# Optimization experiments

Hardware: AMD Instinct MI355X
Metric: run time of the kernel (lower is better)

Reference implementation:

```python
import jax, jax.numpy as jnp
from jax import lax
import numpy as np

BN_EPS = 1e-5

def nearest_resize(x, out_h, out_w):
    # torch F.interpolate(mode='nearest'): src = floor(dst * in / out)
    B, C, H, W = x.shape
    hi = (jnp.arange(out_h) * H) // out_h
    wi = (jnp.arange(out_w) * W) // out_w
    return x[:, :, hi][:, :, :, wi]

def conv1x1(x, w, b=None):
    y = jnp.einsum('bchw,oc->bohw', x, w)
    if b is not None:
        y = y + b[None, :, None, None]
    return y

def dwconv(x, w, stride, pad):
    C = x.shape[1]
    return lax.conv_general_dilated(x, w, (stride, stride), [(pad, pad), (pad, pad)],
                                    dimension_numbers=('NCHW', 'OIHW', 'NCHW'),
                                    feature_group_count=C)

def bn(x, g, b, m, v):
    scale = g / jnp.sqrt(v + BN_EPS)
    return (x - m[None, :, None, None]) * scale[None, :, None, None] + b[None, :, None, None]


def setup_inputs() -> dict:
    key = jax.random.key(0)
    ks = jax.random.split(key, 8)
    B, C, H0, W0 = 4, 512, 192, 192
    w_scale = 0.05
    return {
        'x': jax.random.normal(ks[0], (B, C, H0, W0), jnp.float32),
        'q_w': jax.random.normal(ks[1], (C, C), jnp.float32) * w_scale,
        'q_b': jnp.zeros((C,), jnp.float32),
        'kv_w': jax.random.normal(ks[2], (2 * C, C), jnp.float32) * w_scale,
        'kv_b': jnp.zeros((2 * C,), jnp.float32),
        'sr1_w': jax.random.normal(ks[3], (C, 1, 2, 2), jnp.float32) * w_scale,
        'bn1_g': jnp.ones((C,), jnp.float32),
        'bn1_b': jnp.zeros((C,), jnp.float32),
        'bn1_m': jnp.zeros((C,), jnp.float32),
        'bn1_v': jnp.ones((C,), jnp.float32),
        'sr2_w': jax.random.normal(ks[4], (C, C), jnp.float32) * w_scale,
        'bn2_g': jnp.ones((C,), jnp.float32),
        'bn2_b': jnp.zeros((C,), jnp.float32),
        'bn2_m': jnp.zeros((C,), jnp.float32),
        'bn2_v': jnp.ones((C,), jnp.float32),
        'lc_w': jax.random.normal(ks[5], (C, 1, 3, 3), jnp.float32) * w_scale,
        'lc_b': jnp.zeros((C,), jnp.float32),
        'head_num': 8,
    }


def reference(x, q_w, q_b, kv_w, kv_b, sr1_w, bn1_g, bn1_b, bn1_m, bn1_v,
              sr2_w, bn2_g, bn2_b, bn2_m, bn2_v, lc_w, lc_b, head_num):
    origin_h, origin_w = x.shape[2], x.shape[3]
    x = nearest_resize(x, origin_h // 4, origin_w // 4)
    B, C, H, W = x.shape
    hd = C // head_num
    scale = hd ** (-0.5)

    # q projection (1x1 conv with bias)
    q = conv1x1(x, q_w, q_b)  # [B,C,H,W]

    # spatial reduction: depthwise conv(k=sr, s=sr, p=sr//2) + BN + ReLU, then 1x1 + BN
    sr = sr1_w.shape[-1]
    kv = jax.nn.relu(bn(dwconv(x, sr1_w, sr, sr // 2), bn1_g, bn1_b, bn1_m, bn1_v))
    kv = bn(conv1x1(kv, sr2_w), bn2_g, bn2_b, bn2_m, bn2_v)

    # local depthwise 3x3 conv residual
    kv = dwconv(kv, lc_w, 1, 1) + lc_b[None, :, None, None] + kv

    # kv projection (1x1 conv, 2C output)
    kv = conv1x1(kv, kv_w, kv_b)
    k, v = jnp.split(kv, 2, axis=1)  # each [B,C,Hs,Ws]
    M = k.shape[2] * k.shape[3]

    q_ = jnp.swapaxes(q.reshape(B, head_num, hd, H * W), -1, -2)  # [B,h,N,hd]
    k_ = k.reshape(B, head_num, hd, M)                             # [B,h,hd,M]
    v_ = jnp.swapaxes(v.reshape(B, head_num, hd, M), -1, -2)       # [B,h,M,hd]

    attn = jax.nn.softmax(jnp.matmul(q_, k_) * scale, axis=-1)     # [B,h,N,M]
    out = jnp.swapaxes(jnp.matmul(attn, v_), -1, -2).reshape(B, C, H, W)

    # NOTE: original torch code passes size=(origin_w, origin_h)
    out = nearest_resize(out, origin_w, origin_h)
    return out
```

## Files before the change

### kernel.cpp

```cpp
#include <hip/hip_runtime.h>

#define Bsz 4
#define Cc  512
#define C2  1024
#define H0c 192
#define Hh  48
#define Nn  2304
#define HNh 8
#define HD  64
#define Hs  25
#define Ms  625

typedef const float* fp;
typedef _Float16 f16;
typedef __attribute__((ext_vector_type(8))) _Float16 f16x8;
typedef __attribute__((ext_vector_type(4))) _Float16 f16x4;
typedef __attribute__((ext_vector_type(4))) float    f32x4;

__global__ __launch_bounds__(256) void k_cvtw(fp __restrict__ q_w, fp __restrict__ sr2_w,
                                              fp __restrict__ kv_w, f16* __restrict__ wh) {
    int idx = blockIdx.x * 256 + threadIdx.x;
    float v;
    if (idx < 262144)      v = q_w[idx];
    else if (idx < 524288) v = sr2_w[idx - 262144];
    else                   v = kv_w[idx - 524288];
    wh[idx] = (f16)v;
}

__global__ __launch_bounds__(256) void k_ds_t(fp __restrict__ x,
                                              float* __restrict__ xds,
                                              f16* __restrict__ xt) {
    __shared__ float tile[32][33];
    const int b = blockIdx.z;
    const int s0 = blockIdx.x * 32, r0 = blockIdx.y * 32;
    const int t = threadIdx.x;
    const float* xb = x + (size_t)b * Cc * H0c * H0c;
    float* xdsb = xds + (size_t)b * Cc * Nn;
    #pragma unroll
    for (int p = 0; p < 4; p++) {
        int e = t + p * 256; int i = e >> 5, j = e & 31;
        int c = r0 + i, n = s0 + j;
        float v = xb[((size_t)c * H0c + (n / Hh) * 4) * H0c + (n % Hh) * 4];
        tile[i][j] = v;
        xdsb[(size_t)c * Nn + n] = v;
    }
    __syncthreads();
    #pragma unroll
    for (int p = 0; p < 4; p++) {
        int e = t + p * 256; int oi = e >> 5, oj = e & 31;
        xt[((size_t)b * Nn + s0 + oi) * Cc + r0 + oj] = (f16)tile[oj][oi];
    }
}

__global__ __launch_bounds__(256) void k_sr1t(const float* __restrict__ xds,
                                              fp __restrict__ w, fp g, fp bb, fp bm, fp bv,
                                              f16* __restrict__ kv1t) {
    __shared__ float tile[32][33];
    const int b = blockIdx.z;
    const int s0 = blockIdx.x * 32, r0 = blockIdx.y * 32;
    const int t = threadIdx.x;
    #pragma unroll
    for (int p = 0; p < 4; p++) {
        int e = t + p * 256; int i = e >> 5, j = e & 31;
        int c = r0 + i, n = s0 + j;
        float v = 0.f;
        if (n < Ms) {
            int ho = n / Hs, wo = n % Hs;
            const float* src = xds + ((size_t)b * Cc + c) * Nn;
            float acc = 0.f;
            #pragma unroll
            for (int di = 0; di < 2; di++) {
                int ih = ho * 2 - 1 + di;
                if (ih < 0 || ih >= Hh) continue;
                #pragma unroll
                for (int dj = 0; dj < 2; dj++) {
                    int iw = wo * 2 - 1 + dj;
                    if (iw < 0 || iw >= Hh) continue;
                    acc += w[c * 4 + di * 2 + dj] * src[ih * Hh + iw];
                }
            }
            float sc = g[c] * rsqrtf(bv[c] + 1e-5f);
            v = fmaxf((acc - bm[c]) * sc + bb[c], 0.f);
        }
        tile[i][j] = v;
    }
    __syncthreads();
    #pragma unroll
    for (int p = 0; p < 4; p++) {
        int e = t + p * 256; int oi = e >> 5, oj = e & 31;
        if (s0 + oi < Ms)
            kv1t[((size_t)b * Ms + s0 + oi) * Cc + r0 + oj] = (f16)tile[oj][oi];
    }
}

__global__ __launch_bounds__(256) void k_lct(const float* __restrict__ kv2,
                                             fp __restrict__ w, fp __restrict__ lb,
                                             f16* __restrict__ kv3t) {
    __shared__ float tile[32][33];
    const int b = blockIdx.z;
    const int s0 = blockIdx.x * 32, r0 = blockIdx.y * 32;
    const int t = threadIdx.x;
    #pragma unroll
    for (int p = 0; p < 4; p++) {
        int e = t + p * 256; int i = e >> 5, j = e & 31;
        int c = r0 + i, n = s0 + j;
        float v = 0.f;
        if (n < Ms) {
            int ho = n / Hs, wo = n % Hs;
            const float* src = kv2 + ((size_t)b * Cc + c) * Ms;
            float acc = 0.f;
            #pragma unroll
            for (int di = 0; di < 3; di++) {
                int ih = ho - 1 + di;
                if (ih < 0 || ih >= Hs) continue;
                #pragma unroll
                for (int dj = 0; dj < 3; dj++) {
                    int iw = wo - 1 + dj;
                    if (iw < 0 || iw >= Hs) continue;
                    acc += w[c * 9 + di * 3 + dj] * src[ih * Hs + iw];
                }
            }
            v = acc + lb[c] + src[n];
        }
        tile[i][j] = v;
    }
    __syncthreads();
    #pragma unroll
    for (int p = 0; p < 4; p++) {
        int e = t + p * 256; int oi = e >> 5, oj = e & 31;
        if (s0 + oi < Ms)
            kv3t[((size_t)b * Ms + s0 + oi) * Cc + r0 + oj] = (f16)tile[oj][oi];
    }
}

__global__ __launch_bounds__(256) void k_gemm_mfma(
    const f16* __restrict__ W, const f16* __restrict__ Xt,
    float* __restrict__ Yf, f16* __restrict__ Yt, f16* __restrict__ Vt,
    const int Md, const int Nd, const int NtRows, const int mode, const float oscale,
    fp __restrict__ bias,
    fp __restrict__ bn_g, fp __restrict__ bn_b, fp __restrict__ bn_m, fp __restrict__ bn_v)
{
    __shared__ f16 sA[128 * 80];
    __shared__ f16 sB[128 * 80];
    const int b  = blockIdx.z;
    const int m0 = blockIdx.y * 128, n0 = blockIdx.x * 128;
    const int t = threadIdx.x;
    const int lane = t & 63, w = t >> 6;
    const int lm = lane & 15, q = lane >> 4;
    const int wm = w >> 1, wn = w & 1;
    const f16* Xb = Xt + (size_t)b * Nd * 512;

    f32x4 acc[4][4];
    #pragma unroll
    for (int i = 0; i < 4; i++)
        #pragma unroll
        for (int j = 0; j < 4; j++)
            #pragma unroll
            for (int r = 0; r < 4; r++) acc[i][j][r] = 0.f;

    for (int k0 = 0; k0 < 512; k0 += 64) {
        {
            int r = t >> 1, hh = (t & 1) * 32;
            const f16* wr = W + (size_t)(m0 + r) * 512 + k0 + hh;
            f16* dst = &sA[r * 80 + hh];
            #pragma unroll
            for (int i = 0; i < 4; i++)
                *(f16x8*)&dst[i * 8] = *(const f16x8*)&wr[i * 8];
        }
        {
            int r = t >> 1, hh = (t & 1) * 32;
            bool ok = (n0 + r) < Nd;
            const f16* xr = Xb + (size_t)(n0 + r) * 512 + k0 + hh;
            f16* dst = &sB[r * 80 + hh];
            #pragma unroll
            for (int i = 0; i < 4; i++) {
                f16x8 v;
                if (ok) {
                    v = *(const f16x8*)&xr[i * 8];
                } else {
                    for (int z = 0; z < 8; z++) v[z] = (f16)0.f;
                }
                *(f16x8*)&dst[i * 8] = v;
            }
        }
        __syncthreads();
        #pragma unroll
        for (int ks = 0; ks < 2; ks++) {
            f16x8 af[4], bf[4];
            #pragma unroll
            for (int i = 0; i < 4; i++)
                af[i] = *(const f16x8*)&sA[(wm * 64 + i * 16 + lm) * 80 + ks * 32 + q * 8];
            #pragma unroll
            for (int j = 0; j < 4; j++)
                bf[j] = *(const f16x8*)&sB[(wn * 64 + j * 16 + lm) * 80 + ks * 32 + q * 8];
            #pragma unroll
            for (int i = 0; i < 4; i++)
                #pragma unroll
                for (int j = 0; j < 4; j++)
                    acc[i][j] = __builtin_amdgcn_mfma_f32_16x16x32_f16(af[i], bf[j], acc[i][j], 0, 0, 0);
        }
        __syncthreads();
    }

    #pragma unroll
    for (int i = 0; i < 4; i++) {
        int ob = m0 + wm * 64 + i * 16 + q * 4;
        float badd[4], bsc[4], bsh[4];
        #pragma unroll
        for (int r = 0; r < 4; r++) {
            int o = ob + r;
            badd[r] = bias ? bias[o] : 0.f;
            if (bn_g) { bsc[r] = bn_g[o] * rsqrtf(bn_v[o] + 1e-5f); bsh[r] = bn_b[o] - bn_m[o] * bsc[r]; }
            else      { bsc[r] = 1.f; bsh[r] = 0.f; }
        }
        #pragma unroll
        for (int j = 0; j < 4; j++) {
            int n = n0 + wn * 64 + j * 16 + lm;
            f32x4 a = acc[i][j];
            if (mode == 0) {
                if (n < Nd) {
                    #pragma unroll
                    for (int r = 0; r < 4; r++)
                        Yf[((size_t)b * Md + ob + r) * Nd + n] = (a[r] + badd[r]) * bsc[r] + bsh[r];
                }
            } else if (mode == 1 || (mode == 2 && ob < 512)) {
                f16x4 h;
                #pragma unroll
                for (int r = 0; r < 4; r++) h[r] = (f16)((a[r] + badd[r]) * oscale);
                int hh = ob >> 6, d0 = ob & 63;
                *(f16x4*)&Yt[((size_t)(b * 8 + hh) * NtRows + n) * 64 + d0] = h;
            } else {
                #pragma unroll
                for (int r = 0; r < 4; r++) {
                    float val = (n < Nd) ? (a[r] + badd[r]) : 0.f;
                    Vt[((size_t)b * Cc + (ob + r - 512)) * 640 + n] = (f16)val;
                }
            }
        }
    }
}

__global__ __launch_bounds__(256) void k_attn_mfma(
    const f16* __restrict__ Qt, const f16* __restrict__ Kt,
    const f16* __restrict__ Vt, float* __restrict__ Obuf)
{
    __shared__ f16 sK[64 * 80];
    __shared__ f16 sV[64 * 80];
    __shared__ f16 sP[4][16 * 80];

    int bh = blockIdx.y;
    int n0 = blockIdx.x * 64;
    int t = threadIdx.x, w = t >> 6, lane = t & 63;
    int lm = lane & 15, q = lane >> 4;
    f16* sPw = &sP[w][0];

    f16x8 qf[2];
    {
        const f16* qrow = Qt + ((size_t)bh * Nn + n0 + w * 16 + lm) * 64;
        qf[0] = *(const f16x8*)&qrow[q * 8];
        qf[1] = *(const f16x8*)&qrow[32 + q * 8];
    }

    f32x4 od[4];
    #pragma unroll
    for (int dt = 0; dt < 4; dt++)
        #pragma unroll
        for (int r = 0; r < 4; r++) od[dt][r] = 0.f;
    float mold[4], lold[4];
    #pragma unroll
    for (int r = 0; r < 4; r++) { mold[r] = -1e30f; lold[r] = 0.f; }

    int kr = t >> 2, kc = t & 3;
    const f16* kbase = Kt + (size_t)bh * 640 * 64;
    const f16* vbase = Vt + (size_t)bh * 64 * 640;

    for (int mc = 0; mc < 640; mc += 64) {
        {
            const f16* ksrc = kbase + (size_t)(mc + kr) * 64;
            *(f16x8*)&sK[kr * 80 + kc * 8]      = *(const f16x8*)&ksrc[kc * 8];
            *(f16x8*)&sK[kr * 80 + 32 + kc * 8] = *(const f16x8*)&ksrc[32 + kc * 8];
            const f16* vsrc = vbase + (size_t)kr * 640 + mc;
            *(f16x8*)&sV[kr * 80 + kc * 8]      = *(const f16x8*)&vsrc[kc * 8];
            *(f16x8*)&sV[kr * 80 + 32 + kc * 8] = *(const f16x8*)&vsrc[32 + kc * 8];
        }
        __syncthreads();

        f32x4 sc4[4];
        #pragma unroll
        for (int j = 0; j < 4; j++)
            #pragma unroll
            for (int r = 0; r < 4; r++) sc4[j][r] = 0.f;
        #pragma unroll
        for (int ks = 0; ks < 2; ks++) {
            #pragma unroll
            for (int j = 0; j < 4; j++) {
                f16x8 kf = *(const f16x8*)&sK[(j * 16 + lm) * 80 + ks * 32 + q * 8];
                sc4[j] = __builtin_amdgcn_mfma_f32_16x16x32_f16(qf[ks], kf, sc4[j], 0, 0, 0);
            }
        }

        const bool lastc = (mc >= 576);
        #pragma unroll
        for (int reg = 0; reg < 4; reg++) {
            float mx;
            if (lastc) {
                mx = -1e30f;
                #pragma unroll
                for (int j = 0; j < 4; j++) {
                    float s = sc4[j][reg];
                    if (576 + j * 16 + lm >= Ms) s = -1e30f;
                    sc4[j][reg] = s;
                    mx = fmaxf(mx, s);
                }
            } else {
                mx = fmaxf(fmaxf(sc4[0][reg], sc4[1][reg]),
                           fmaxf(sc4[2][reg], sc4[3][reg]));
            }
            #pragma unroll
            for (int off = 1; off < 16; off <<= 1) mx = fmaxf(mx, __shfl_xor(mx, off));
            float mnew = fmaxf(mold[reg], mx);
            float alpha = __expf(mold[reg] - mnew);
            float rs = 0.f;
            #pragma unroll
            for (int j = 0; j < 4; j++) {
                float p = __expf(sc4[j][reg] - mnew);
                sc4[j][reg] = p;
                rs += p;
            }
            #pragma unroll
            for (int off = 1; off < 16; off <<= 1) rs += __shfl_xor(rs, off);
            lold[reg] = lold[reg] * alpha + rs;
            mold[reg] = mnew;
            #pragma unroll
            for (int dt = 0; dt < 4; dt++) od[dt][reg] *= alpha;
            #pragma unroll
            for (int j = 0; j < 4; j++)
                sPw[(q * 4 + reg) * 80 + j * 16 + lm] = (f16)sc4[j][reg];
        }

        #pragma unroll
        for (int ks = 0; ks < 2; ks++) {
            f16x8 pa = *(const f16x8*)&sPw[lm * 80 + ks * 32 + q * 8];
            #pragma unroll
            for (int dt = 0; dt < 4; dt++) {
                f16x8 vf = *(const f16x8*)&sV[(dt * 16 + lm) * 80 + ks * 32 + q * 8];
                od[dt] = __builtin_amdgcn_mfma_f32_16x16x32_f16(pa, vf, od[dt], 0, 0, 0);
            }
        }
        __syncthreads();
    }

    float inv[4];
    #pragma unroll
    for (int r = 0; r < 4; r++) inv[r] = 1.f / lold[r];
    #pragma unroll
    for (int dt = 0; dt < 4; dt++) {
        f32x4 o;
        #pragma unroll
        for (int r = 0; r < 4; r++) o[r] = od[dt][r] * inv[r];
        size_t c = (size_t)bh * 64 + dt * 16 + lm;
        *(f32x4*)&Obuf[c * Nn + n0 + w * 16 + q * 4] = o;
    }
}

__global__ __launch_bounds__(256) void k_upsample(const float* __restrict__ O,
                                                  float* __restrict__ out) {
    size_t idx = (size_t)blockIdx.x * 256 + threadIdx.x;
    if (idx >= (size_t)Bsz * Cc * H0c * 48) return;
    int jg = (int)(idx % 48);
    int i  = (int)((idx / 48) % H0c);
    int bc = (int)(idx / ((size_t)48 * H0c));
    float s = O[(size_t)bc * Nn + (i >> 2) * Hh + jg];
    float4 pack = make_float4(s, s, s, s);
    *(float4*)(out + ((size_t)bc * H0c + i) * H0c + jg * 4) = pack;
}

extern "C" void kernel_launch(void* const* d_in, const int* in_sizes, int n_in,
                              void* d_out, int out_size, void* d_ws, size_t ws_size,
                              hipStream_t stream) {
    (void)in_sizes; (void)n_in; (void)out_size; (void)ws_size;
    fp x     = (fp)d_in[0];
    fp q_w   = (fp)d_in[1];
    fp q_b   = (fp)d_in[2];
    fp kv_w  = (fp)d_in[3];
    fp kv_b  = (fp)d_in[4];
    fp sr1_w = (fp)d_in[5];
    fp bn1_g = (fp)d_in[6];
    fp bn1_b = (fp)d_in[7];
    fp bn1_m = (fp)d_in[8];
    fp bn1_v = (fp)d_in[9];
    fp sr2_w = (fp)d_in[10];
    fp bn2_g = (fp)d_in[11];
    fp bn2_b = (fp)d_in[12];
    fp bn2_m = (fp)d_in[13];
    fp bn2_v = (fp)d_in[14];
    fp lc_w  = (fp)d_in[15];
    fp lc_b  = (fp)d_in[16];
    float* out = (float*)d_out;

    float* ws   = (float*)d_ws;
    float* xds  = ws;
    float* Obuf = ws;
    float* kv2  = ws + 4718592;
    f16*   Kt   = (f16*)(ws + 5998592);
    f16*   vt   = (f16*)(ws + 6653952);
    f16*   xt   = (f16*)(ws + 7309312);
    f16*   kv1t = xt;
    f16*   kv3t = xt;
    f16*   Qt   = (f16*)(ws + 9668608);
    f16*   wh   = (f16*)(ws + 12027904);

    k_cvtw<<<4096, 256, 0, stream>>>(q_w, sr2_w, kv_w, wh);
    k_ds_t<<<dim3(72, 16, Bsz), 256, 0, stream>>>(x, xds, xt);
    k_gemm_mfma<<<dim3(18, 4, Bsz), 256, 0, stream>>>(wh, xt, nullptr, Qt, nullptr,
        Cc, Nn, Nn, 1, 0.125f, q_b, nullptr, nullptr, nullptr, nullptr);
    k_sr1t<<<dim3(20, 16, Bsz), 256, 0, stream>>>(xds, sr1_w, bn1_g, bn1_b, bn1_m, bn1_v, kv1t);
    k_gemm_mfma<<<dim3(5, 4, Bsz), 256, 0, stream>>>(wh + 262144, kv1t, kv2, nullptr, nullptr,
        Cc, Ms, 0, 0, 1.f, nullptr, bn2_g, bn2_b, bn2_m, bn2_v);
    k_lct<<<dim3(20, 16, Bsz), 256, 0, stream>>>(kv2, lc_w, lc_b, kv3t);
    k_gemm_mfma<<<dim3(5, 8, Bsz), 256, 0, stream>>>(wh + 524288, kv3t, nullptr, Kt, vt,
        C2, Ms, 640, 2, 1.f, kv_b, nullptr, nullptr, nullptr, nullptr);
    k_attn_mfma<<<dim3(Nn / 64, Bsz * HNh), 256, 0, stream>>>(Qt, Kt, vt, Obuf);
    k_upsample<<<(unsigned)((size_t)Bsz * Cc * H0c * 48 / 256), 256, 0, stream>>>(Obuf, out);
}
```

Measured before the change: 617.2 us.

## Merge front-end kernels and co-launch Q and SR2 GEMMs, drop xds buffer

Three kernels become one launch: the weight fp16 conversion (now float4-vectorized), the downsample-transpose, and the SR1 depthwise+BN+ReLU. SR1 now reads directly from the strided full-resolution x, so the fp32 downsampled intermediate no longer needs to be written and read back. The Q projection GEMM and the SR2 GEMM are fused into a single launch with a flattened block index, so the small SR2 GEMM overlaps the larger one. The upsample kernel becomes a grid-stride loop over 2048 blocks, and the workspace is relaid out because kv1t no longer aliases xt. The SR1 path's strided gathers from x may be less cache-friendly than reading the compact intermediate.

```diff
diff --git a/kernel.cpp b/kernel.cpp
--- a/kernel.cpp
+++ b/kernel.cpp
@@ -17,79 +17,81 @@
 typedef __attribute__((ext_vector_type(4))) _Float16 f16x4;
 typedef __attribute__((ext_vector_type(4))) float    f32x4;
 
-__global__ __launch_bounds__(256) void k_cvtw(fp __restrict__ q_w, fp __restrict__ sr2_w,
-                                              fp __restrict__ kv_w, f16* __restrict__ wh) {
-    int idx = blockIdx.x * 256 + threadIdx.x;
-    float v;
-    if (idx < 262144)      v = q_w[idx];
-    else if (idx < 524288) v = sr2_w[idx - 262144];
-    else                   v = kv_w[idx - 524288];
-    wh[idx] = (f16)v;
-}
-
-__global__ __launch_bounds__(256) void k_ds_t(fp __restrict__ x,
-                                              float* __restrict__ xds,
-                                              f16* __restrict__ xt) {
+__global__ __launch_bounds__(256) void k_front(
+    fp __restrict__ x, f16* __restrict__ xt, f16* __restrict__ kv1t,
+    fp __restrict__ w1, fp g, fp bb, fp bm, fp bv,
+    fp __restrict__ q_w, fp __restrict__ sr2_w, fp __restrict__ kv_w,
+    f16* __restrict__ wh)
+{
     __shared__ float tile[32][33];
-    const int b = blockIdx.z;
-    const int s0 = blockIdx.x * 32, r0 = blockIdx.y * 32;
     const int t = threadIdx.x;
-    const float* xb = x + (size_t)b * Cc * H0c * H0c;
-    float* xdsb = xds + (size_t)b * Cc * Nn;
-    #pragma unroll
-    for (int p = 0; p < 4; p++) {
-        int e = t + p * 256; int i = e >> 5, j = e & 31;
-        int c = r0 + i, n = s0 + j;
-        float v = xb[((size_t)c * H0c + (n / Hh) * 4) * H0c + (n % Hh) * 4];
-        tile[i][j] = v;
-        xdsb[(size_t)c * Nn + n] = v;
-    }
-    __syncthreads();
-    #pragma unroll
-    for (int p = 0; p < 4; p++) {
-        int e = t + p * 256; int oi = e >> 5, oj = e & 31;
-        xt[((size_t)b * Nn + s0 + oi) * Cc + r0 + oj] = (f16)tile[oj][oi];
-    }
-}
-
-__global__ __launch_bounds__(256) void k_sr1t(const float* __restrict__ xds,
-                                              fp __restrict__ w, fp g, fp bb, fp bm, fp bv,
-                                              f16* __restrict__ kv1t) {
-    __shared__ float tile[32][33];
-    const int b = blockIdx.z;
-    const int s0 = blockIdx.x * 32, r0 = blockIdx.y * 32;
-    const int t = threadIdx.x;
-    #pragma unroll
-    for (int p = 0; p < 4; p++) {
-        int e = t + p * 256; int i = e >> 5, j = e & 31;
-        int c = r0 + i, n = s0 + j;
-        float v = 0.f;
-        if (n < Ms) {
-            int ho = n / Hs, wo = n % Hs;
-            const float* src = xds + ((size_t)b * Cc + c) * Nn;
-            float acc = 0.f;
-            #pragma unroll
-            for (int di = 0; di < 2; di++) {
-                int ih = ho * 2 - 1 + di;
-                if (ih < 0 || ih >= Hh) continue;
-                #pragma unroll
-                for (int dj = 0; dj < 2; dj++) {
-                    int iw = wo * 2 - 1 + dj;
-                    if (iw < 0 || iw >= Hh) continue;
-                    acc += w[c * 4 + di * 2 + dj] * src[ih * Hh + iw];
-                }
-            }
-            float sc = g[c] * rsqrtf(bv[c] + 1e-5f);
-            v = fmaxf((acc - bm[c]) * sc + bb[c], 0.f);
-        }
-        tile[i][j] = v;
-    }
-    __syncthreads();
-    #pragma unroll
-    for (int p = 0; p < 4; p++) {
-        int e = t + p * 256; int oi = e >> 5, oj = e & 31;
-        if (s0 + oi < Ms)
-            kv1t[((size_t)b * Ms + s0 + oi) * Cc + r0 + oj] = (f16)tile[oj][oi];
+    int bid = blockIdx.x;
+
+    if (bid < 4608) {
+        const int b  = bid / 1152;
+        const int yi = (bid / 72) % 16;
+        const int xi = bid % 72;
+        const int s0 = xi * 32, r0 = yi * 32;
+        const float* xb = x + (size_t)b * Cc * H0c * H0c;
+        #pragma unroll
+        for (int p = 0; p < 4; p++) {
+            int e = t + p * 256; int i = e >> 5, j = e & 31;
+            int c = r0 + i, n = s0 + j;
+            tile[i][j] = xb[((size_t)c * H0c + (n / Hh) * 4) * H0c + (n % Hh) * 4];
+        }
+        __syncthreads();
+        #pragma unroll
+        for (int p = 0; p < 4; p++) {
+            int e = t + p * 256; int oi = e >> 5, oj = e & 31;
+            xt[((size_t)b * Nn + s0 + oi) * Cc + r0 + oj] = (f16)tile[oj][oi];
+        }
+    } else if (bid < 5888) {
+        bid -= 4608;
+        const int b  = bid / 320;
+        const int yi = (bid / 20) % 16;
+        const int xi = bid % 20;
+        const int s0 = xi * 32, r0 = yi * 32;
+        #pragma unroll
+        for (int p = 0; p < 4; p++) {
+            int e = t + p * 256; int i = e >> 5, j = e & 31;
+            int c = r0 + i, n = s0 + j;
+            float v = 0.f;
+            if (n < Ms) {
+                int ho = n / Hs, wo = n % Hs;
+                const float* src = x + (size_t)(b * Cc + c) * H0c * H0c;
+                float acc = 0.f;
+                #pragma unroll
+                for (int di = 0; di < 2; di++) {
+                    int ih = ho * 2 - 1 + di;
+                    if (ih < 0 || ih >= Hh) continue;
+                    #pragma unroll
+                    for (int dj = 0; dj < 2; dj++) {
+                        int iw = wo * 2 - 1 + dj;
+                        if (iw < 0 || iw >= Hh) continue;
+                        acc += w1[c * 4 + di * 2 + dj] * src[(size_t)(ih * 4) * H0c + iw * 4];
+                    }
+                }
+                float sc = g[c] * rsqrtf(bv[c] + 1e-5f);
+                v = fmaxf((acc - bm[c]) * sc + bb[c], 0.f);
+            }
+            tile[i][j] = v;
+        }
+        __syncthreads();
+        #pragma unroll
+        for (int p = 0; p < 4; p++) {
+            int e = t + p * 256; int oi = e >> 5, oj = e & 31;
+            if (s0 + oi < Ms)
+                kv1t[((size_t)b * Ms + s0 + oi) * Cc + r0 + oj] = (f16)tile[oj][oi];
+        }
+    } else {
+        bid -= 5888;
+        int i4 = (bid * 256 + t) * 4;
+        float4 v;
+        if (i4 < 262144)      v = *(const float4*)&q_w[i4];
+        else if (i4 < 524288) v = *(const float4*)&sr2_w[i4 - 262144];
+        else                  v = *(const float4*)&kv_w[i4 - 524288];
+        f16x4 h; h[0] = (f16)v.x; h[1] = (f16)v.y; h[2] = (f16)v.z; h[3] = (f16)v.w;
+        *(f16x4*)&wh[i4] = h;
     }
 }
 
@@ -130,6 +132,112 @@
         int e = t + p * 256; int oi = e >> 5, oj = e & 31;
         if (s0 + oi < Ms)
             kv3t[((size_t)b * Ms + s0 + oi) * Cc + r0 + oj] = (f16)tile[oj][oi];
+    }
+}
+
+__device__ __forceinline__ void gemm_body(
+    const f16* __restrict__ W, const f16* __restrict__ Xt,
+    float* __restrict__ Yf, f16* __restrict__ Yt, f16* __restrict__ Vt,
+    const int Md, const int Nd, const int NtRows, const int mode, const float oscale,
+    fp __restrict__ bias,
+    fp __restrict__ bn_g, fp __restrict__ bn_b, fp __restrict__ bn_m, fp __restrict__ bn_v,
+    const int bx, const int by, const int bz, f16* sA, f16* sB)
+{
+    const int b  = bz;
+    const int m0 = by * 128, n0 = bx * 128;
+    const int t = threadIdx.x;
+    const int lane = t & 63, w = t >> 6;
+    const int lm = lane & 15, q = lane >> 4;
+    const int wm = w >> 1, wn = w & 1;
+    const f16* Xb = Xt + (size_t)b * Nd * 512;
+
+    f32x4 acc[4][4];
+    #pragma unroll
+    for (int i = 0; i < 4; i++)
+        #pragma unroll
+        for (int j = 0; j < 4; j++)
+            #pragma unroll
+            for (int r = 0; r < 4; r++) acc[i][j][r] = 0.f;
+
+    for (int k0 = 0; k0 < 512; k0 += 64) {
+        {
+            int r = t >> 1, hh = (t & 1) * 32;
+            const f16* wr = W + (size_t)(m0 + r) * 512 + k0 + hh;
+            f16* dst = &sA[r * 80 + hh];
+            #pragma unroll
+            for (int i = 0; i < 4; i++)
+                *(f16x8*)&dst[i * 8] = *(const f16x8*)&wr[i * 8];
+        }
+        {
+            int r = t >> 1, hh = (t & 1) * 32;
+            bool ok = (n0 + r) < Nd;
+            const f16* xr = Xb + (size_t)(n0 + r) * 512 + k0 + hh;
+            f16* dst = &sB[r * 80 + hh];
+            #pragma unroll
+            for (int i = 0; i < 4; i++) {
+                f16x8 v;
+                if (ok) {
+                    v = *(const f16x8*)&xr[i * 8];
+                } else {
+                    for (int z = 0; z < 8; z++) v[z] = (f16)0.f;
+                }
+                *(f16x8*)&dst[i * 8] = v;
+            }
+        }
+        __syncthreads();
+        #pragma unroll
+        for (int ks = 0; ks < 2; ks++) {
+            f16x8 af[4], bf[4];
+            #pragma unroll
+            for (int i = 0; i < 4; i++)
+                af[i] = *(const f16x8*)&sA[(wm * 64 + i * 16 + lm) * 80 + ks * 32 + q * 8];
+            #pragma unroll
+            for (int j = 0; j < 4; j++)
+                bf[j] = *(const f16x8*)&sB[(wn * 64 + j * 16 + lm) * 80 + ks * 32 + q * 8];
+            #pragma unroll
+            for (int i = 0; i < 4; i++)
+                #pragma unroll
+                for (int j = 0; j < 4; j++)
+                    acc[i][j] = __builtin_amdgcn_mfma_f32_16x16x32_f16(af[i], bf[j], acc[i][j], 0, 0, 0);
+        }
+        __syncthreads();
+    }
+
+    #pragma unroll
+    for (int i = 0; i < 4; i++) {
+        int ob = m0 + wm * 64 + i * 16 + q * 4;
+        float badd[4], bsc[4], bsh[4];
+        #pragma unroll
+        for (int r = 0; r < 4; r++) {
+            int o = ob + r;
+            badd[r] = bias ? bias[o] : 0.f;
+            if (bn_g) { bsc[r] = bn_g[o] * rsqrtf(bn_v[o] + 1e-5f); bsh[r] = bn_b[o] - bn_m[o] * bsc[r]; }
+            else      { bsc[r] = 1.f; bsh[r] = 0.f; }
+        }
+        #pragma unroll
+        for (int j = 0; j < 4; j++) {
+            int n = n0 + wn * 64 + j * 16 + lm;
+            f32x4 a = acc[i][j];
+            if (mode == 0) {
+                if (n < Nd) {
+                    #pragma unroll
+                    for (int r = 0; r < 4; r++)
+                        Yf[((size_t)b * Md + ob + r) * Nd + n] = (a[r] + badd[r]) * bsc[r] + bsh[r];
+                }
+            } else if (mode == 1 || (mode == 2 && ob < 512)) {
+                f16x4 h;
+                #pragma unroll
+                for (int r = 0; r < 4; r++) h[r] = (f16)((a[r] + badd[r]) * oscale);
+                int hh = ob >> 6, d0 = ob & 63;
+                *(f16x4*)&Yt[((size_t)(b * 8 + hh) * NtRows + n) * 64 + d0] = h;
+            } else {
+                #pragma unroll
+                for (int r = 0; r < 4; r++) {
+                    float val = (n < Nd) ? (a[r] + badd[r]) : 0.f;
+                    Vt[((size_t)b * Cc + (ob + r - 512)) * 640 + n] = (f16)val;
+                }
+            }
+        }
     }
 }
 
@@ -142,101 +250,29 @@
 {
     __shared__ f16 sA[128 * 80];
     __shared__ f16 sB[128 * 80];
-    const int b  = blockIdx.z;
-    const int m0 = blockIdx.y * 128, n0 = blockIdx.x * 128;
-    const int t = threadIdx.x;
-    const int lane = t & 63, w = t >> 6;
-    const int lm = lane & 15, q = lane >> 4;
-    const int wm = w >> 1, wn = w & 1;
-    const f16* Xb = Xt + (size_t)b * Nd * 512;
-
-    f32x4 acc[4][4];
-    #pragma unroll
-    for (int i = 0; i < 4; i++)
-        #pragma unroll
-        for (int j = 0; j < 4; j++)
-            #pragma unroll
-            for (int r = 0; r < 4; r++) acc[i][j][r] = 0.f;
-
-    for (int k0 = 0; k0 < 512; k0 += 64) {
-        {
-            int r = t >> 1, hh = (t & 1) * 32;
-            const f16* wr = W + (size_t)(m0 + r) * 512 + k0 + hh;
-            f16* dst = &sA[r * 80 + hh];
-            #pragma unroll
-            for (int i = 0; i < 4; i++)
-                *(f16x8*)&dst[i * 8] = *(const f16x8*)&wr[i * 8];
-        }
-        {
-            int r = t >> 1, hh = (t & 1) * 32;
-            bool ok = (n0 + r) < Nd;
-            const f16* xr = Xb + (size_t)(n0 + r) * 512 + k0 + hh;
-            f16* dst = &sB[r * 80 + hh];
-            #pragma unroll
-            for (int i = 0; i < 4; i++) {
-                f16x8 v;
-                if (ok) {
-                    v = *(const f16x8*)&xr[i * 8];
-                } else {
-                    for (int z = 0; z < 8; z++) v[z] = (f16)0.f;
-                }
-                *(f16x8*)&dst[i * 8] = v;
-            }
-        }
-        __syncthreads();
-        #pragma unroll
-        for (int ks = 0; ks < 2; ks++) {
-            f16x8 af[4], bf[4];
-            #pragma unroll
-            for (int i = 0; i < 4; i++)
-                af[i] = *(const f16x8*)&sA[(wm * 64 + i * 16 + lm) * 80 + ks * 32 + q * 8];
-            #pragma unroll
-            for (int j = 0; j < 4; j++)
-                bf[j] = *(const f16x8*)&sB[(wn * 64 + j * 16 + lm) * 80 + ks * 32 + q * 8];
-            #pragma unroll
-            for (int i = 0; i < 4; i++)
-                #pragma unroll
-                for (int j = 0; j < 4; j++)
-                    acc[i][j] = __builtin_amdgcn_mfma_f32_16x16x32_f16(af[i], bf[j], acc[i][j], 0, 0, 0);
-        }
-        __syncthreads();
-    }
-
-    #pragma unroll
-    for (int i = 0; i < 4; i++) {
-        int ob = m0 + wm * 64 + i * 16 + q * 4;
-        float badd[4], bsc[4], bsh[4];
-        #pragma unroll
-        for (int r = 0; r < 4; r++) {
-            int o = ob + r;
-            badd[r] = bias ? bias[o] : 0.f;
-            if (bn_g) { bsc[r] = bn_g[o] * rsqrtf(bn_v[o] + 1e-5f); bsh[r] = bn_b[o] - bn_m[o] * bsc[r]; }
-            else      { bsc[r] = 1.f; bsh[r] = 0.f; }
-        }
-        #pragma unroll
-        for (int j = 0; j < 4; j++) {
-            int n = n0 + wn * 64 + j * 16 + lm;
-            f32x4 a = acc[i][j];
-            if (mode == 0) {
-                if (n < Nd) {
-                    #pragma unroll
-                    for (int r = 0; r < 4; r++)
-                        Yf[((size_t)b * Md + ob + r) * Nd + n] = (a[r] + badd[r]) * bsc[r] + bsh[r];
-                }
-            } else if (mode == 1 || (mode == 2 && ob < 512)) {
-                f16x4 h;
-                #pragma unroll
-                for (int r = 0; r < 4; r++) h[r] = (f16)((a[r] + badd[r]) * oscale);
-                int hh = ob >> 6, d0 = ob & 63;
-                *(f16x4*)&Yt[((size_t)(b * 8 + hh) * NtRows + n) * 64 + d0] = h;
-            } else {
-                #pragma unroll
-                for (int r = 0; r < 4; r++) {
-                    float val = (n < Nd) ? (a[r] + badd[r]) : 0.f;
-                    Vt[((size_t)b * Cc + (ob + r - 512)) * 640 + n] = (f16)val;
-                }
-            }
-        }
+    gemm_body(W, Xt, Yf, Yt, Vt, Md, Nd, NtRows, mode, oscale,
+              bias, bn_g, bn_b, bn_m, bn_v,
+              blockIdx.x, blockIdx.y, blockIdx.z, sA, sB);
+}
+
+__global__ __launch_bounds__(256) void k_gemm2(
+    const f16* __restrict__ W0, const f16* __restrict__ X0, f16* __restrict__ Yt0,
+    const float osc0, fp __restrict__ bias0,
+    const f16* __restrict__ W1, const f16* __restrict__ X1, float* __restrict__ Yf1,
+    fp g1, fp b1, fp m1, fp v1)
+{
+    __shared__ f16 sA[128 * 80];
+    __shared__ f16 sB[128 * 80];
+    int bid = blockIdx.x;
+    if (bid < 288) {
+        int bx = bid % 18, by = (bid / 18) % 4, bz = bid / 72;
+        gemm_body(W0, X0, nullptr, Yt0, nullptr, Cc, Nn, Nn, 1, osc0,
+                  bias0, nullptr, nullptr, nullptr, nullptr, bx, by, bz, sA, sB);
+    } else {
+        bid -= 288;
+        int bx = bid % 5, by = (bid / 5) % 4, bz = bid / 20;
+        gemm_body(W1, X1, Yf1, nullptr, nullptr, Cc, Ms, 0, 0, 1.f,
+                  nullptr, g1, b1, m1, v1, bx, by, bz, sA, sB);
     }
 }
 
@@ -365,14 +401,16 @@
 
 __global__ __launch_bounds__(256) void k_upsample(const float* __restrict__ O,
                                                   float* __restrict__ out) {
-    size_t idx = (size_t)blockIdx.x * 256 + threadIdx.x;
-    if (idx >= (size_t)Bsz * Cc * H0c * 48) return;
-    int jg = (int)(idx % 48);
-    int i  = (int)((idx / 48) % H0c);
-    int bc = (int)(idx / ((size_t)48 * H0c));
-    float s = O[(size_t)bc * Nn + (i >> 2) * Hh + jg];
-    float4 pack = make_float4(s, s, s, s);
-    *(float4*)(out + ((size_t)bc * H0c + i) * H0c + jg * 4) = pack;
+    const size_t total = (size_t)Bsz * Cc * H0c * 48;
+    for (size_t idx = (size_t)blockIdx.x * 256 + threadIdx.x; idx < total;
+         idx += (size_t)gridDim.x * 256) {
+        int jg = (int)(idx % 48);
+        int i  = (int)((idx / 48) % H0c);
+        int bc = (int)(idx / ((size_t)48 * H0c));
+        float s = O[(size_t)bc * Nn + (i >> 2) * Hh + jg];
+        float4 pack = make_float4(s, s, s, s);
+        *(float4*)(out + ((size_t)bc * H0c + i) * H0c + jg * 4) = pack;
+    }
 }
 
 extern "C" void kernel_launch(void* const* d_in, const int* in_sizes, int n_in,
@@ -399,27 +437,23 @@
     float* out = (float*)d_out;
 
     float* ws   = (float*)d_ws;
-    float* xds  = ws;
+    f16*   xt   = (f16*)ws;
+    f16*   kv1t = (f16*)(ws + 2359296);
+    f16*   wh   = (f16*)(ws + 2999296);
+    float* kv2  = ws + 3523584;
     float* Obuf = ws;
-    float* kv2  = ws + 4718592;
-    f16*   Kt   = (f16*)(ws + 5998592);
-    f16*   vt   = (f16*)(ws + 6653952);
-    f16*   xt   = (f16*)(ws + 7309312);
-    f16*   kv1t = xt;
-    f16*   kv3t = xt;
-    f16*   Qt   = (f16*)(ws + 9668608);
-    f16*   wh   = (f16*)(ws + 12027904);
-
-    k_cvtw<<<4096, 256, 0, stream>>>(q_w, sr2_w, kv_w, wh);
-    k_ds_t<<<dim3(72, 16, Bsz), 256, 0, stream>>>(x, xds, xt);
-    k_gemm_mfma<<<dim3(18, 4, Bsz), 256, 0, stream>>>(wh, xt, nullptr, Qt, nullptr,
-        Cc, Nn, Nn, 1, 0.125f, q_b, nullptr, nullptr, nullptr, nullptr);
-    k_sr1t<<<dim3(20, 16, Bsz), 256, 0, stream>>>(xds, sr1_w, bn1_g, bn1_b, bn1_m, bn1_v, kv1t);
-    k_gemm_mfma<<<dim3(5, 4, Bsz), 256, 0, stream>>>(wh + 262144, kv1t, kv2, nullptr, nullptr,
-        Cc, Ms, 0, 0, 1.f, nullptr, bn2_g, bn2_b, bn2_m, bn2_v);
+    f16*   Qt   = (f16*)(ws + 4803584);
+    f16*   Kt   = (f16*)(ws + 7162880);
+    f16*   vt   = (f16*)(ws + 7818240);
+    f16*   kv3t = (f16*)(ws + 8473600);
+
+    k_front<<<6912, 256, 0, stream>>>(x, xt, kv1t, sr1_w, bn1_g, bn1_b, bn1_m, bn1_v,
+                                      q_w, sr2_w, kv_w, wh);
+    k_gemm2<<<368, 256, 0, stream>>>(wh, xt, Qt, 0.125f, q_b,
+                                     wh + 262144, kv1t, kv2, bn2_g, bn2_b, bn2_m, bn2_v);
     k_lct<<<dim3(20, 16, Bsz), 256, 0, stream>>>(kv2, lc_w, lc_b, kv3t);
     k_gemm_mfma<<<dim3(5, 8, Bsz), 256, 0, stream>>>(wh + 524288, kv3t, nullptr, Kt, vt,
         C2, Ms, 640, 2, 1.f, kv_b, nullptr, nullptr, nullptr, nullptr);
     k_attn_mfma<<<dim3(Nn / 64, Bsz * HNh), 256, 0, stream>>>(Qt, Kt, vt, Obuf);
-    k_upsample<<<(unsigned)((size_t)Bsz * Cc * H0c * 48 / 256), 256, 0, stream>>>(Obuf, out);
-}
+    k_upsample<<<2048, 256, 0, stream>>>(Obuf, out);
+}
```

Measured after the change: 603.2 us. -2.3%, faster.
